# Performance work log

Measured on AMD Instinct MI355X. Metric: run time of the kernel, lower is better.

## Reference

```python
import jax, jax.numpy as jnp
import numpy as np

N_NODES = 50000
N_EDGES = 800000
D = 128            # in_channels == hidden_channels
N_LAYERS = 3
OUT = 16
N_GRAPHS = 128


def setup_inputs() -> dict:
    key = jax.random.key(0)
    ks = jax.random.split(key, 12)
    x = jax.random.normal(ks[0], (N_NODES, D), dtype=jnp.float32)
    edge_index = jax.random.randint(ks[1], (2, N_EDGES), 0, N_NODES, dtype=jnp.int64)
    batch_ids = jnp.sort(jax.random.randint(ks[2], (N_NODES,), 0, N_GRAPHS, dtype=jnp.int64))
    s = 1.0 / np.sqrt(D)
    # Stacked per-layer GraphConv weights (all layers are D->D here).
    Wrel = jax.random.uniform(ks[3], (N_LAYERS, D, D), jnp.float32, -s, s)
    brel = jax.random.uniform(ks[4], (N_LAYERS, D), jnp.float32, -s, s)
    Wroot = jax.random.uniform(ks[5], (N_LAYERS, D, D), jnp.float32, -s, s)
    # post_mp MLP head
    W1 = jax.random.uniform(ks[6], (D, D), jnp.float32, -s, s)
    b1 = jax.random.uniform(ks[7], (D,), jnp.float32, -s, s)
    W2 = jax.random.uniform(ks[8], (D, OUT), jnp.float32, -s, s)
    b2 = jax.random.uniform(ks[9], (OUT,), jnp.float32, -s, s)
    return {"x": x, "edge_index": edge_index, "batch_ids": batch_ids,
            "Wrel": Wrel, "brel": brel, "Wroot": Wroot,
            "W1": W1, "b1": b1, "W2": W2, "b2": b2}


def reference(x, edge_index, batch_ids, Wrel, brel, Wroot, W1, b1, W2, b2):
    src, dst = edge_index[0], edge_index[1]
    h = x
    for l in range(N_LAYERS):
        # GraphConv: lin_rel(sum_{j->i} h_j) + lin_root(h_i)
        agg = jax.ops.segment_sum(h[src], dst, num_segments=N_NODES)  # [N, D]
        h = agg @ Wrel[l] + brel[l] + h @ Wroot[l]
        h = jax.nn.relu(h)
        # dropout p=0.0 / eval mode -> identity
    # global mean pool over graphs
    sums = jax.ops.segment_sum(h, batch_ids, num_segments=N_GRAPHS)          # [G, D]
    counts = jax.ops.segment_sum(jnp.ones((N_NODES,), h.dtype), batch_ids,
                                 num_segments=N_GRAPHS)                       # [G]
    pooled = sums / jnp.maximum(counts, 1.0)[:, None]
    # post_mp MLP (dropout identity in eval)
    out = (pooled @ W1 + b1) @ W2 + b2                                        # [G, OUT]
    return out
```

## Files before the change

kernel.cpp:

```cpp
#include <hip/hip_runtime.h>

#define N_NODES 50000
#define N_EDGES 800000
#define D 128
#define N_LAYERS 3
#define OUT_F 16
#define N_GRAPHS 128
#define NBUCK 391
#define EPB 4096
#define NB3 ((N_EDGES + EPB - 1) / EPB)
#define CAP 4096
#define NT32 ((N_NODES + 31) / 32)
#define PITCH 132
#define NCAST 6250
#define NPREPW 96

typedef __attribute__((ext_vector_type(8))) short short8;
typedef __attribute__((ext_vector_type(16))) float floatx16;

__device__ __forceinline__ unsigned short f2bf(float f) {
  unsigned int u = __float_as_uint(f);
  u += 0x7fff + ((u >> 16) & 1);
  return (unsigned short)(u >> 16);
}
__device__ __forceinline__ float bf2f(unsigned short b) {
  return __uint_as_float(((unsigned int)b) << 16);
}
__device__ __forceinline__ float blo(unsigned v) { return __uint_as_float(v << 16); }
__device__ __forceinline__ float bhi(unsigned v) { return __uint_as_float(v & 0xffff0000u); }

__global__ __launch_bounds__(256) void partition_kernel(
    const int* __restrict__ src, const int* __restrict__ dst,
    int* __restrict__ cursor, unsigned* __restrict__ pairs) {
  __shared__ unsigned pk[EPB];
  __shared__ int hist[NBUCK];
  __shared__ int wcur[NBUCK];
  const int e0 = blockIdx.x * EPB;
  const int n = min(EPB, N_EDGES - e0);
  const int t = threadIdx.x;
  for (int i = t; i < NBUCK; i += 256) hist[i] = 0;
  __syncthreads();
  for (int i = t; i < n; i += 256) {
    int d = dst[e0 + i], s = src[e0 + i];
    pk[i] = ((unsigned)d << 16) | (unsigned)s;
    atomicAdd(&hist[d >> 7], 1);
  }
  __syncthreads();
  for (int i = t; i < NBUCK; i += 256)
    wcur[i] = i * CAP + (hist[i] ? atomicAdd(&cursor[i], hist[i]) : 0);
  __syncthreads();
  for (int i = t; i < n; i += 256) {
    unsigned p = pk[i];
    int pos = atomicAdd(&wcur[p >> 23], 1);
    pairs[pos] = p;
  }
}

__global__ __launch_bounds__(256) void bucket_sort_kernel(
    const unsigned* __restrict__ pairs, const int* __restrict__ cursor,
    int* __restrict__ rowbeg, int* __restrict__ rowend, int* __restrict__ esrc) {
  __shared__ unsigned pk[CAP];
  __shared__ int sorted[CAP];
  __shared__ int hist[128], off[128], cur[128];
  const int bkt = blockIdx.x;
  const int t = threadIdx.x;
  const int beg = bkt * CAP;
  const int cnt = cursor[bkt];
  if (t < 128) hist[t] = 0;
  __syncthreads();
  for (int i = t; i < cnt; i += 256) {
    unsigned p = pairs[beg + i];
    pk[i] = p;
    atomicAdd(&hist[(p >> 16) & 127], 1);
  }
  __syncthreads();
  if (t < 128) off[t] = hist[t];
  __syncthreads();
  for (int o = 1; o < 128; o <<= 1) {
    int x = (t < 128 && t >= o) ? off[t - o] : 0;
    __syncthreads();
    if (t < 128) off[t] += x;
    __syncthreads();
  }
  if (t < 128) {
    int node = bkt * 128 + t;
    if (node < N_NODES) {
      rowbeg[node] = beg + off[t] - hist[t];
      rowend[node] = beg + off[t];
    }
    cur[t] = off[t] - hist[t];
  }
  __syncthreads();
  for (int i = t; i < cnt; i += 256) {
    unsigned p = pk[i];
    int pos = atomicAdd(&cur[(p >> 16) & 127], 1);
    sorted[pos] = (int)(p & 0xFFFFu);
  }
  __syncthreads();
  for (int i = t; i < cnt; i += 256) esrc[beg + i] = sorted[i];
}

__global__ __launch_bounds__(256) void prep_all_kernel(
    const float* __restrict__ x, unsigned short* __restrict__ x16,
    const float* __restrict__ Wrel, const float* __restrict__ Wroot,
    unsigned short* __restrict__ wt, int* __restrict__ cursor) {
  const int bid = blockIdx.x;
  const int t = threadIdx.x;
  if (bid < NCAST) {
    const int i = bid * 256 + t;
    const float4 v = *(const float4*)&x[(size_t)i * 4];
    uint2 o;
    o.x = f2bf(v.x) | ((unsigned)f2bf(v.y) << 16);
    o.y = f2bf(v.z) | ((unsigned)f2bf(v.w) << 16);
    *(uint2*)&x16[(size_t)i * 4] = o;
  } else if (bid < NCAST + NPREPW) {
    const int idx = (bid - NCAST) * 256 + t;
    const int lane = idx & 63;
    const int kst = (idx >> 6) & 31;
    const int nt = (idx >> 11) & 1;
    const int half = (idx >> 12) & 1;
    const int l = idx >> 13;
    const int n = half * 64 + nt * 32 + (lane & 31);
    const int kx0 = kst * 16 + (lane >> 5) * 8;
    const int seg = kx0 >> 7;
    const int k0 = kx0 & 127;
    const int mat = seg >> 1, lo = seg & 1;
    const float* W = (mat ? Wroot : Wrel) + (size_t)l * D * D;
    unsigned short v[8];
#pragma unroll
    for (int j = 0; j < 8; ++j) {
      float w = W[(size_t)(k0 + j) * D + n];
      unsigned short hi = f2bf(w);
      v[j] = lo ? f2bf(w - bf2f(hi)) : hi;
    }
    unsigned short* dstp =
        wt + ((size_t)l * 128 + (half * 2 + nt) * 32 + kst) * 512 + lane * 8;
    *(uint4*)dstp = *(const uint4*)v;
  } else {
    const int i = (bid - NCAST - NPREPW) * 256 + t;
    if (i < NBUCK) cursor[i] = 0;
  }
}

__global__ __launch_bounds__(512, 8) void layer_kernel(
    const unsigned short* __restrict__ h,
    const int* __restrict__ rowbeg, const int* __restrict__ rowend,
    const int* __restrict__ esrc,
    const unsigned short* __restrict__ wt,
    const float* __restrict__ brel,
    unsigned short* __restrict__ outp) {
  __shared__ unsigned short atile[32 * PITCH];
  __shared__ unsigned short htile[32 * PITCH];
  __shared__ float redB[4][16][64];
  const int t = threadIdx.x;
  const int r0 = blockIdx.x * 32;
  const int g = t >> 4, li = t & 15;
  const int row = r0 + g;
  const unsigned short* hp = h + (size_t)li * 8;

  if (row < N_NODES) {
    *(uint4*)&htile[g * PITCH + li * 8] =
        *(const uint4*)&h[(size_t)row * D + li * 8];
  } else {
    const uint4 z = {0, 0, 0, 0};
    *(uint4*)&htile[g * PITCH + li * 8] = z;
  }

  int beg = 0, end = 0;
  if (row < N_NODES) { beg = rowbeg[row]; end = rowend[row]; }
  float a0 = 0, a1 = 0, a2 = 0, a3 = 0, a4 = 0, a5 = 0, a6 = 0, a7 = 0;
  int e = beg;
  for (; e + 4 <= end; e += 4) {
    const int s0 = esrc[e],     s1 = esrc[e + 1];
    const int s2 = esrc[e + 2], s3 = esrc[e + 3];
    const uint4 v0 = *(const uint4*)&hp[(size_t)s0 * D];
    const uint4 v1 = *(const uint4*)&hp[(size_t)s1 * D];
    const uint4 v2 = *(const uint4*)&hp[(size_t)s2 * D];
    const uint4 v3 = *(const uint4*)&hp[(size_t)s3 * D];
    a0 += blo(v0.x) + blo(v1.x) + blo(v2.x) + blo(v3.x);
    a1 += bhi(v0.x) + bhi(v1.x) + bhi(v2.x) + bhi(v3.x);
    a2 += blo(v0.y) + blo(v1.y) + blo(v2.y) + blo(v3.y);
    a3 += bhi(v0.y) + bhi(v1.y) + bhi(v2.y) + bhi(v3.y);
    a4 += blo(v0.z) + blo(v1.z) + blo(v2.z) + blo(v3.z);
    a5 += bhi(v0.z) + bhi(v1.z) + bhi(v2.z) + bhi(v3.z);
    a6 += blo(v0.w) + blo(v1.w) + blo(v2.w) + blo(v3.w);
    a7 += bhi(v0.w) + bhi(v1.w) + bhi(v2.w) + bhi(v3.w);
  }
  for (; e < end; ++e) {
    const uint4 v0 = *(const uint4*)&hp[(size_t)esrc[e] * D];
    a0 += blo(v0.x); a1 += bhi(v0.x);
    a2 += blo(v0.y); a3 += bhi(v0.y);
    a4 += blo(v0.z); a5 += bhi(v0.z);
    a6 += blo(v0.w); a7 += bhi(v0.w);
  }
  {
    uint4 o;
    o.x = f2bf(a0) | ((unsigned)f2bf(a1) << 16);
    o.y = f2bf(a2) | ((unsigned)f2bf(a3) << 16);
    o.z = f2bf(a4) | ((unsigned)f2bf(a5) << 16);
    o.w = f2bf(a6) | ((unsigned)f2bf(a7) << 16);
    *(uint4*)&atile[g * PITCH + li * 8] = o;
  }
  __syncthreads();

  const int wave = t >> 6, lane = t & 63;
  const int p = wave & 3, chain = wave >> 2;
  const int r2 = lane & 31, hseg = lane >> 5;
  const unsigned short* tile = chain ? htile : atile;
  short8 fr[8];
#pragma unroll
  for (int i = 0; i < 8; ++i)
    fr[i] = *(const short8*)&tile[r2 * PITCH + i * 16 + hseg * 8];
  const unsigned short* ws = wt + (size_t)(p * 32 + chain * 16) * 512;
  floatx16 acc = {0.f};
#pragma unroll
  for (int k = 0; k < 16; ++k) {
    const short8 b = *(const short8*)&ws[(size_t)k * 512 + lane * 8];
    acc = __builtin_amdgcn_mfma_f32_32x32x16_bf16(fr[k & 7], b, acc, 0, 0, 0);
  }
  if (chain) {
#pragma unroll
    for (int reg = 0; reg < 16; ++reg) redB[p][reg][lane] = acc[reg];
  }
  __syncthreads();
  if (!chain) {
    const int cb = p * 32 + r2;
    const float bias = brel[cb];
#pragma unroll
    for (int reg = 0; reg < 16; ++reg) {
      const int orow = r0 + (reg & 3) + 8 * (reg >> 2) + 4 * hseg;
      if (orow < N_NODES)
        outp[(size_t)orow * D + cb] =
            f2bf(fmaxf(acc[reg] + redB[p][reg][lane] + bias, 0.f));
    }
  }
}

__device__ __forceinline__ int lb_search(const int* __restrict__ a, int n, int key) {
  int lo = 0, hi = n;
  while (lo < hi) {
    int m = (lo + hi) >> 1;
    if (a[m] < key) lo = m + 1; else hi = m;
  }
  return lo;
}

__global__ __launch_bounds__(256) void pool_head_kernel(
    const unsigned short* __restrict__ h, const int* __restrict__ batch,
    const float* __restrict__ W1, const float* __restrict__ b1,
    const float* __restrict__ W2, const float* __restrict__ b2,
    float* __restrict__ out) {
  __shared__ float sums_lds[16][128];
  __shared__ float pooled[128];
  __shared__ float hidden[128];
  __shared__ int range[2];
  const int g = blockIdx.x;
  const int t = threadIdx.x;
  if (t < 2) range[t] = lb_search(batch, N_NODES, g + t);
  __syncthreads();
  const int lo = range[0], hi = range[1];
  const int rg = t >> 4, cg = t & 15;
  float a0 = 0, a1 = 0, a2 = 0, a3 = 0, a4 = 0, a5 = 0, a6 = 0, a7 = 0;
  for (int n = lo + rg; n < hi; n += 16) {
    const uint4 v = *(const uint4*)&h[(size_t)n * D + cg * 8];
    a0 += blo(v.x); a1 += bhi(v.x);
    a2 += blo(v.y); a3 += bhi(v.y);
    a4 += blo(v.z); a5 += bhi(v.z);
    a6 += blo(v.w); a7 += bhi(v.w);
  }
  sums_lds[rg][cg * 8 + 0] = a0; sums_lds[rg][cg * 8 + 1] = a1;
  sums_lds[rg][cg * 8 + 2] = a2; sums_lds[rg][cg * 8 + 3] = a3;
  sums_lds[rg][cg * 8 + 4] = a4; sums_lds[rg][cg * 8 + 5] = a5;
  sums_lds[rg][cg * 8 + 6] = a6; sums_lds[rg][cg * 8 + 7] = a7;
  __syncthreads();
  if (t < 128) {
    float s = 0.f;
#pragma unroll
    for (int r = 0; r < 16; ++r) s += sums_lds[r][t];
    pooled[t] = s / fmaxf((float)(hi - lo), 1.f);
  }
  __syncthreads();
  if (t < 128) {
    float a = b1[t];
    for (int k = 0; k < D; ++k) a += pooled[k] * W1[k * D + t];
    hidden[t] = a;
  }
  __syncthreads();
  if (t < OUT_F) {
    float o = b2[t];
    for (int k = 0; k < D; ++k) o += hidden[k] * W2[k * OUT_F + t];
    out[(size_t)g * OUT_F + t] = o;
  }
}

extern "C" void kernel_launch(void* const* d_in, const int* in_sizes, int n_in,
                              void* d_out, int out_size, void* d_ws, size_t ws_size,
                              hipStream_t stream) {
  const float* x     = (const float*)d_in[0];
  const int*   ei    = (const int*)d_in[1];
  const int*   batch = (const int*)d_in[2];
  const float* Wrel  = (const float*)d_in[3];
  const float* brel  = (const float*)d_in[4];
  const float* Wroot = (const float*)d_in[5];
  const float* W1    = (const float*)d_in[6];
  const float* b1    = (const float*)d_in[7];
  const float* W2    = (const float*)d_in[8];
  const float* b2    = (const float*)d_in[9];
  float* out = (float*)d_out;

  const size_t ND = (size_t)N_NODES * D;
  unsigned short* bufA = (unsigned short*)d_ws;
  unsigned short* bufB = bufA + ND;
  unsigned short* bufC = bufB + ND;
  unsigned short* wt   = bufC + ND;
  int* rowbeg = (int*)(wt + (size_t)N_LAYERS * 128 * 512);
  int* rowend = rowbeg + N_NODES;
  int* esrc   = rowend + N_NODES;
  unsigned* pairs = (unsigned*)(esrc + (size_t)NBUCK * CAP);
  int* cursor = (int*)(pairs + (size_t)NBUCK * CAP);

  const int* esrc_in = ei;
  const int* edst_in = ei + N_EDGES;

  prep_all_kernel<<<NCAST + NPREPW + 2, 256, 0, stream>>>(
      x, bufC, Wrel, Wroot, wt, cursor);
  partition_kernel<<<NB3, 256, 0, stream>>>(esrc_in, edst_in, cursor, pairs);
  bucket_sort_kernel<<<NBUCK, 256, 0, stream>>>(pairs, cursor, rowbeg, rowend, esrc);

  const size_t WL = (size_t)128 * 512;
  layer_kernel<<<NT32, 512, 0, stream>>>(bufC, rowbeg, rowend, esrc,
                                         wt, brel, bufA);
  layer_kernel<<<NT32, 512, 0, stream>>>(bufA, rowbeg, rowend, esrc,
                                         wt + WL, brel + D, bufB);
  layer_kernel<<<NT32, 512, 0, stream>>>(bufB, rowbeg, rowend, esrc,
                                         wt + 2 * WL, brel + 2 * D, bufA);

  pool_head_kernel<<<N_GRAPHS, 256, 0, stream>>>(bufA, batch, W1, b1, W2, b2, out);
}
```

Baseline: 264.1 us.

## Split layer into XCD-sliced gather kernel and separate GEMM kernel

The fused gather+GEMM layer kernel becomes two kernels. A new aggregation kernel has each block handle one 32-column slice of the feature dimension, chosen from the block id so that blocks on the same XCD read the same slice. This is meant to keep each XCD's gathered working set in its own L2. The aggregated bf16 rows go through global memory to a separate MFMA GEMM kernel, which adds an extra write and read of the N×D tensor plus extra kernel launches per layer.

```diff
diff --git a/kernel.cpp b/kernel.cpp
--- a/kernel.cpp
+++ b/kernel.cpp
@@ -14,6 +14,7 @@
 #define PITCH 132
 #define NCAST 6250
 #define NPREPW 96
+#define NHB 782
 
 typedef __attribute__((ext_vector_type(8))) short short8;
 typedef __attribute__((ext_vector_type(16))) float floatx16;
@@ -142,34 +143,22 @@
   }
 }
 
-__global__ __launch_bounds__(512, 8) void layer_kernel(
+__global__ __launch_bounds__(256, 8) void agg_kernel(
     const unsigned short* __restrict__ h,
     const int* __restrict__ rowbeg, const int* __restrict__ rowend,
-    const int* __restrict__ esrc,
-    const unsigned short* __restrict__ wt,
-    const float* __restrict__ brel,
-    unsigned short* __restrict__ outp) {
-  __shared__ unsigned short atile[32 * PITCH];
-  __shared__ unsigned short htile[32 * PITCH];
-  __shared__ float redB[4][16][64];
-  const int t = threadIdx.x;
-  const int r0 = blockIdx.x * 32;
-  const int g = t >> 4, li = t & 15;
-  const int row = r0 + g;
-  const unsigned short* hp = h + (size_t)li * 8;
-
-  if (row < N_NODES) {
-    *(uint4*)&htile[g * PITCH + li * 8] =
-        *(const uint4*)&h[(size_t)row * D + li * 8];
-  } else {
-    const uint4 z = {0, 0, 0, 0};
-    *(uint4*)&htile[g * PITCH + li * 8] = z;
-  }
-
-  int beg = 0, end = 0;
-  if (row < N_NODES) { beg = rowbeg[row]; end = rowend[row]; }
+    const int* __restrict__ esrc, unsigned short* __restrict__ agg) {
+  const int bid = blockIdx.x;
+  const int xcd = bid & 7;
+  const int slice = xcd >> 1;
+  const int bh = (bid >> 3) * 2 + (xcd & 1);
+  const int t = threadIdx.x;
+  const int g = t >> 2, li = t & 3;
+  const int node = bh * 64 + g;
+  if (node >= N_NODES) return;
+  const unsigned short* hp = h + slice * 32 + li * 8;
+  int e = rowbeg[node];
+  const int end = rowend[node];
   float a0 = 0, a1 = 0, a2 = 0, a3 = 0, a4 = 0, a5 = 0, a6 = 0, a7 = 0;
-  int e = beg;
   for (; e + 4 <= end; e += 4) {
     const int s0 = esrc[e],     s1 = esrc[e + 1];
     const int s2 = esrc[e + 2], s3 = esrc[e + 3];
@@ -193,13 +182,35 @@
     a4 += blo(v0.z); a5 += bhi(v0.z);
     a6 += blo(v0.w); a7 += bhi(v0.w);
   }
-  {
-    uint4 o;
-    o.x = f2bf(a0) | ((unsigned)f2bf(a1) << 16);
-    o.y = f2bf(a2) | ((unsigned)f2bf(a3) << 16);
-    o.z = f2bf(a4) | ((unsigned)f2bf(a5) << 16);
-    o.w = f2bf(a6) | ((unsigned)f2bf(a7) << 16);
-    *(uint4*)&atile[g * PITCH + li * 8] = o;
+  uint4 o;
+  o.x = f2bf(a0) | ((unsigned)f2bf(a1) << 16);
+  o.y = f2bf(a2) | ((unsigned)f2bf(a3) << 16);
+  o.z = f2bf(a4) | ((unsigned)f2bf(a5) << 16);
+  o.w = f2bf(a6) | ((unsigned)f2bf(a7) << 16);
+  *(uint4*)&agg[(size_t)node * D + slice * 32 + li * 8] = o;
+}
+
+__global__ __launch_bounds__(512, 8) void gemm_kernel(
+    const unsigned short* __restrict__ agg, const unsigned short* __restrict__ hv,
+    const unsigned short* __restrict__ wt,
+    const float* __restrict__ brel,
+    unsigned short* __restrict__ outp) {
+  __shared__ unsigned short atile[32 * PITCH];
+  __shared__ unsigned short htile[32 * PITCH];
+  __shared__ float redB[4][16][64];
+  const int t = threadIdx.x;
+  const int r0 = blockIdx.x * 32;
+  const int g = t >> 4, li = t & 15;
+  const int row = r0 + g;
+  if (row < N_NODES) {
+    *(uint4*)&htile[g * PITCH + li * 8] =
+        *(const uint4*)&hv[(size_t)row * D + li * 8];
+    *(uint4*)&atile[g * PITCH + li * 8] =
+        *(const uint4*)&agg[(size_t)row * D + li * 8];
+  } else {
+    const uint4 z = {0, 0, 0, 0};
+    *(uint4*)&htile[g * PITCH + li * 8] = z;
+    *(uint4*)&atile[g * PITCH + li * 8] = z;
   }
   __syncthreads();
 
@@ -328,12 +339,13 @@
   bucket_sort_kernel<<<NBUCK, 256, 0, stream>>>(pairs, cursor, rowbeg, rowend, esrc);
 
   const size_t WL = (size_t)128 * 512;
-  layer_kernel<<<NT32, 512, 0, stream>>>(bufC, rowbeg, rowend, esrc,
-                                         wt, brel, bufA);
-  layer_kernel<<<NT32, 512, 0, stream>>>(bufA, rowbeg, rowend, esrc,
-                                         wt + WL, brel + D, bufB);
-  layer_kernel<<<NT32, 512, 0, stream>>>(bufB, rowbeg, rowend, esrc,
-                                         wt + 2 * WL, brel + 2 * D, bufA);
+  const int agg_blocks = NHB * 8;
+  agg_kernel<<<agg_blocks, 256, 0, stream>>>(bufC, rowbeg, rowend, esrc, bufB);
+  gemm_kernel<<<NT32, 512, 0, stream>>>(bufB, bufC, wt, brel, bufA);
+  agg_kernel<<<agg_blocks, 256, 0, stream>>>(bufA, rowbeg, rowend, esrc, bufB);
+  gemm_kernel<<<NT32, 512, 0, stream>>>(bufB, bufA, wt + WL, brel + D, bufC);
+  agg_kernel<<<agg_blocks, 256, 0, stream>>>(bufC, rowbeg, rowend, esrc, bufB);
+  gemm_kernel<<<NT32, 512, 0, stream>>>(bufB, bufC, wt + 2 * WL, brel + 2 * D, bufA);
 
   pool_head_kernel<<<N_GRAPHS, 256, 0, stream>>>(bufA, batch, W1, b1, W2, b2, out);
 }
```

Measured after the change: 322.6 us. 1.22x slower.

## Fuse edge partition into prep kernel, unroll gather by 8, relax launch bounds

Applied to the files above, without the earlier changes.

Merges the edge-partition work into the bf16 cast and weight-packing prep kernel, so one launch covers all three jobs, and moves cursor zeroing to a hipMemsetAsync. The neighbor gather in the layer kernel gains an 8-wide unrolled loop to keep more loads in flight. The layer kernel's launch-bound occupancy hint drops from 8 to 4, which allows more registers per thread but fewer resident waves. The fused kernel carries the partition's LDS footprint into every cast block, which may reduce occupancy for the cast work.

```diff
diff --git a/kernel.cpp b/kernel.cpp
--- a/kernel.cpp
+++ b/kernel.cpp
@@ -29,92 +29,45 @@
 __device__ __forceinline__ float blo(unsigned v) { return __uint_as_float(v << 16); }
 __device__ __forceinline__ float bhi(unsigned v) { return __uint_as_float(v & 0xffff0000u); }
 
-__global__ __launch_bounds__(256) void partition_kernel(
+__global__ __launch_bounds__(256) void prep_part_kernel(
     const int* __restrict__ src, const int* __restrict__ dst,
-    int* __restrict__ cursor, unsigned* __restrict__ pairs) {
+    int* __restrict__ cursor, unsigned* __restrict__ pairs,
+    const float* __restrict__ x, unsigned short* __restrict__ x16,
+    const float* __restrict__ Wrel, const float* __restrict__ Wroot,
+    unsigned short* __restrict__ wt) {
   __shared__ unsigned pk[EPB];
   __shared__ int hist[NBUCK];
   __shared__ int wcur[NBUCK];
-  const int e0 = blockIdx.x * EPB;
-  const int n = min(EPB, N_EDGES - e0);
-  const int t = threadIdx.x;
-  for (int i = t; i < NBUCK; i += 256) hist[i] = 0;
-  __syncthreads();
-  for (int i = t; i < n; i += 256) {
-    int d = dst[e0 + i], s = src[e0 + i];
-    pk[i] = ((unsigned)d << 16) | (unsigned)s;
-    atomicAdd(&hist[d >> 7], 1);
-  }
-  __syncthreads();
-  for (int i = t; i < NBUCK; i += 256)
-    wcur[i] = i * CAP + (hist[i] ? atomicAdd(&cursor[i], hist[i]) : 0);
-  __syncthreads();
-  for (int i = t; i < n; i += 256) {
-    unsigned p = pk[i];
-    int pos = atomicAdd(&wcur[p >> 23], 1);
-    pairs[pos] = p;
-  }
-}
-
-__global__ __launch_bounds__(256) void bucket_sort_kernel(
-    const unsigned* __restrict__ pairs, const int* __restrict__ cursor,
-    int* __restrict__ rowbeg, int* __restrict__ rowend, int* __restrict__ esrc) {
-  __shared__ unsigned pk[CAP];
-  __shared__ int sorted[CAP];
-  __shared__ int hist[128], off[128], cur[128];
-  const int bkt = blockIdx.x;
-  const int t = threadIdx.x;
-  const int beg = bkt * CAP;
-  const int cnt = cursor[bkt];
-  if (t < 128) hist[t] = 0;
-  __syncthreads();
-  for (int i = t; i < cnt; i += 256) {
-    unsigned p = pairs[beg + i];
-    pk[i] = p;
-    atomicAdd(&hist[(p >> 16) & 127], 1);
-  }
-  __syncthreads();
-  if (t < 128) off[t] = hist[t];
-  __syncthreads();
-  for (int o = 1; o < 128; o <<= 1) {
-    int x = (t < 128 && t >= o) ? off[t - o] : 0;
-    __syncthreads();
-    if (t < 128) off[t] += x;
-    __syncthreads();
-  }
-  if (t < 128) {
-    int node = bkt * 128 + t;
-    if (node < N_NODES) {
-      rowbeg[node] = beg + off[t] - hist[t];
-      rowend[node] = beg + off[t];
-    }
-    cur[t] = off[t] - hist[t];
-  }
-  __syncthreads();
-  for (int i = t; i < cnt; i += 256) {
-    unsigned p = pk[i];
-    int pos = atomicAdd(&cur[(p >> 16) & 127], 1);
-    sorted[pos] = (int)(p & 0xFFFFu);
-  }
-  __syncthreads();
-  for (int i = t; i < cnt; i += 256) esrc[beg + i] = sorted[i];
-}
-
-__global__ __launch_bounds__(256) void prep_all_kernel(
-    const float* __restrict__ x, unsigned short* __restrict__ x16,
-    const float* __restrict__ Wrel, const float* __restrict__ Wroot,
-    unsigned short* __restrict__ wt, int* __restrict__ cursor) {
   const int bid = blockIdx.x;
   const int t = threadIdx.x;
-  if (bid < NCAST) {
-    const int i = bid * 256 + t;
+  if (bid < NB3) {
+    const int e0 = bid * EPB;
+    const int n = min(EPB, N_EDGES - e0);
+    for (int i = t; i < NBUCK; i += 256) hist[i] = 0;
+    __syncthreads();
+    for (int i = t; i < n; i += 256) {
+      int d = dst[e0 + i], s = src[e0 + i];
+      pk[i] = ((unsigned)d << 16) | (unsigned)s;
+      atomicAdd(&hist[d >> 7], 1);
+    }
+    __syncthreads();
+    for (int i = t; i < NBUCK; i += 256)
+      wcur[i] = i * CAP + (hist[i] ? atomicAdd(&cursor[i], hist[i]) : 0);
+    __syncthreads();
+    for (int i = t; i < n; i += 256) {
+      unsigned p = pk[i];
+      int pos = atomicAdd(&wcur[p >> 23], 1);
+      pairs[pos] = p;
+    }
+  } else if (bid < NB3 + NCAST) {
+    const int i = (bid - NB3) * 256 + t;
     const float4 v = *(const float4*)&x[(size_t)i * 4];
     uint2 o;
     o.x = f2bf(v.x) | ((unsigned)f2bf(v.y) << 16);
     o.y = f2bf(v.z) | ((unsigned)f2bf(v.w) << 16);
     *(uint2*)&x16[(size_t)i * 4] = o;
-  } else if (bid < NCAST + NPREPW) {
-    const int idx = (bid - NCAST) * 256 + t;
+  } else {
+    const int idx = (bid - NB3 - NCAST) * 256 + t;
     const int lane = idx & 63;
     const int kst = (idx >> 6) & 31;
     const int nt = (idx >> 11) & 1;
@@ -136,13 +89,54 @@
     unsigned short* dstp =
         wt + ((size_t)l * 128 + (half * 2 + nt) * 32 + kst) * 512 + lane * 8;
     *(uint4*)dstp = *(const uint4*)v;
-  } else {
-    const int i = (bid - NCAST - NPREPW) * 256 + t;
-    if (i < NBUCK) cursor[i] = 0;
-  }
-}
-
-__global__ __launch_bounds__(512, 8) void layer_kernel(
+  }
+}
+
+__global__ __launch_bounds__(256) void bucket_sort_kernel(
+    const unsigned* __restrict__ pairs, const int* __restrict__ cursor,
+    int* __restrict__ rowbeg, int* __restrict__ rowend, int* __restrict__ esrc) {
+  __shared__ unsigned pk[CAP];
+  __shared__ int sorted[CAP];
+  __shared__ int hist[128], off[128], cur[128];
+  const int bkt = blockIdx.x;
+  const int t = threadIdx.x;
+  const int beg = bkt * CAP;
+  const int cnt = cursor[bkt];
+  if (t < 128) hist[t] = 0;
+  __syncthreads();
+  for (int i = t; i < cnt; i += 256) {
+    unsigned p = pairs[beg + i];
+    pk[i] = p;
+    atomicAdd(&hist[(p >> 16) & 127], 1);
+  }
+  __syncthreads();
+  if (t < 128) off[t] = hist[t];
+  __syncthreads();
+  for (int o = 1; o < 128; o <<= 1) {
+    int x = (t < 128 && t >= o) ? off[t - o] : 0;
+    __syncthreads();
+    if (t < 128) off[t] += x;
+    __syncthreads();
+  }
+  if (t < 128) {
+    int node = bkt * 128 + t;
+    if (node < N_NODES) {
+      rowbeg[node] = beg + off[t] - hist[t];
+      rowend[node] = beg + off[t];
+    }
+    cur[t] = off[t] - hist[t];
+  }
+  __syncthreads();
+  for (int i = t; i < cnt; i += 256) {
+    unsigned p = pk[i];
+    int pos = atomicAdd(&cur[(p >> 16) & 127], 1);
+    sorted[pos] = (int)(p & 0xFFFFu);
+  }
+  __syncthreads();
+  for (int i = t; i < cnt; i += 256) esrc[beg + i] = sorted[i];
+}
+
+__global__ __launch_bounds__(512, 4) void layer_kernel(
     const unsigned short* __restrict__ h,
     const int* __restrict__ rowbeg, const int* __restrict__ rowend,
     const int* __restrict__ esrc,
@@ -170,6 +164,36 @@
   if (row < N_NODES) { beg = rowbeg[row]; end = rowend[row]; }
   float a0 = 0, a1 = 0, a2 = 0, a3 = 0, a4 = 0, a5 = 0, a6 = 0, a7 = 0;
   int e = beg;
+  for (; e + 8 <= end; e += 8) {
+    const int s0 = esrc[e],     s1 = esrc[e + 1];
+    const int s2 = esrc[e + 2], s3 = esrc[e + 3];
+    const int s4 = esrc[e + 4], s5 = esrc[e + 5];
+    const int s6 = esrc[e + 6], s7 = esrc[e + 7];
+    const uint4 v0 = *(const uint4*)&hp[(size_t)s0 * D];
+    const uint4 v1 = *(const uint4*)&hp[(size_t)s1 * D];
+    const uint4 v2 = *(const uint4*)&hp[(size_t)s2 * D];
+    const uint4 v3 = *(const uint4*)&hp[(size_t)s3 * D];
+    const uint4 v4 = *(const uint4*)&hp[(size_t)s4 * D];
+    const uint4 v5 = *(const uint4*)&hp[(size_t)s5 * D];
+    const uint4 v6 = *(const uint4*)&hp[(size_t)s6 * D];
+    const uint4 v7 = *(const uint4*)&hp[(size_t)s7 * D];
+    a0 += (blo(v0.x) + blo(v1.x) + blo(v2.x) + blo(v3.x)) +
+          (blo(v4.x) + blo(v5.x) + blo(v6.x) + blo(v7.x));
+    a1 += (bhi(v0.x) + bhi(v1.x) + bhi(v2.x) + bhi(v3.x)) +
+          (bhi(v4.x) + bhi(v5.x) + bhi(v6.x) + bhi(v7.x));
+    a2 += (blo(v0.y) + blo(v1.y) + blo(v2.y) + blo(v3.y)) +
+          (blo(v4.y) + blo(v5.y) + blo(v6.y) + blo(v7.y));
+    a3 += (bhi(v0.y) + bhi(v1.y) + bhi(v2.y) + bhi(v3.y)) +
+          (bhi(v4.y) + bhi(v5.y) + bhi(v6.y) + bhi(v7.y));
+    a4 += (blo(v0.z) + blo(v1.z) + blo(v2.z) + blo(v3.z)) +
+          (blo(v4.z) + blo(v5.z) + blo(v6.z) + blo(v7.z));
+    a5 += (bhi(v0.z) + bhi(v1.z) + bhi(v2.z) + bhi(v3.z)) +
+          (bhi(v4.z) + bhi(v5.z) + bhi(v6.z) + bhi(v7.z));
+    a6 += (blo(v0.w) + blo(v1.w) + blo(v2.w) + blo(v3.w)) +
+          (blo(v4.w) + blo(v5.w) + blo(v6.w) + blo(v7.w));
+    a7 += (bhi(v0.w) + bhi(v1.w) + bhi(v2.w) + bhi(v3.w)) +
+          (bhi(v4.w) + bhi(v5.w) + bhi(v6.w) + bhi(v7.w));
+  }
   for (; e + 4 <= end; e += 4) {
     const int s0 = esrc[e],     s1 = esrc[e + 1];
     const int s2 = esrc[e + 2], s3 = esrc[e + 3];
@@ -322,9 +346,9 @@
   const int* esrc_in = ei;
   const int* edst_in = ei + N_EDGES;
 
-  prep_all_kernel<<<NCAST + NPREPW + 2, 256, 0, stream>>>(
-      x, bufC, Wrel, Wroot, wt, cursor);
-  partition_kernel<<<NB3, 256, 0, stream>>>(esrc_in, edst_in, cursor, pairs);
+  hipMemsetAsync(cursor, 0, NBUCK * sizeof(int), stream);
+  prep_part_kernel<<<NB3 + NCAST + NPREPW, 256, 0, stream>>>(
+      esrc_in, edst_in, cursor, pairs, x, bufC, Wrel, Wroot, wt);
   bucket_sort_kernel<<<NBUCK, 256, 0, stream>>>(pairs, cursor, rowbeg, rowend, esrc);
 
   const size_t WL = (size_t)128 * 512;
```

Result: slower. 275.7 us (+4.4%).
